# Kernel tuning notes

Hardware: AMD Instinct MI355X
Metric: run time of the kernel (lower is better)

The kernel has to match this reference:

```python
import jax, jax.numpy as jnp
import numpy as np

N_EMBED = 256
N_HEAD = 8
HEAD = N_EMBED // N_HEAD
LN_EPS = 1e-5


def _layernorm(x, g, b):
    mu = jnp.mean(x, axis=-1, keepdims=True)
    var = jnp.mean(jnp.square(x - mu), axis=-1, keepdims=True)
    return (x - mu) * jax.lax.rsqrt(var + LN_EPS) * g + b


def setup_inputs() -> dict:
    key = jax.random.key(0)
    ks = jax.random.split(key, 12)
    B, T, C, H, D = 16, 1024, N_EMBED, N_HEAD, HEAD
    s = C ** -0.5
    return {
        "x": jax.random.normal(ks[0], (B, T, C), jnp.float32),
        "wq": jax.random.normal(ks[1], (H, C, D), jnp.float32) * s,
        "wk": jax.random.normal(ks[2], (H, C, D), jnp.float32) * s,
        "wv": jax.random.normal(ks[3], (H, C, D), jnp.float32) * s,
        "w_proj": jax.random.normal(ks[4], (C, C), jnp.float32) * s,
        "b_proj": jnp.zeros((C,), jnp.float32),
        "w1": jax.random.normal(ks[5], (C, 4 * C), jnp.float32) * s,
        "b1": jnp.zeros((4 * C,), jnp.float32),
        "w2": jax.random.normal(ks[6], (4 * C, C), jnp.float32) * (4 * C) ** -0.5,
        "b2": jnp.zeros((C,), jnp.float32),
        "ln1_g": jnp.ones((C,), jnp.float32),
        "ln1_b": jnp.zeros((C,), jnp.float32),
        "ln2_g": jnp.ones((C,), jnp.float32),
        "ln2_b": jnp.zeros((C,), jnp.float32),
    }


def reference(x, wq, wk, wv, w_proj, b_proj, w1, b1, w2, b2,
              ln1_g, ln1_b, ln2_g, ln2_b):
    B, T, C = x.shape
    # --- multi-head causal self-attention on ln1(x) ---
    h = _layernorm(x, ln1_g, ln1_b)
    q = jnp.einsum('btc,hcd->bhtd', h, wq)
    k = jnp.einsum('btc,hcd->bhtd', h, wk)
    v = jnp.einsum('btc,hcd->bhtd', h, wv)
    # NOTE: original scales by n_embed**-0.5 (C of input), not head_size
    wei = jnp.einsum('bhtd,bhsd->bhts', q, k) * (C ** -0.5)
    causal = jnp.tril(jnp.ones((T, T), bool))
    wei = jnp.where(causal, wei, -jnp.inf)
    wei = jax.nn.softmax(wei, axis=-1)
    att = jnp.einsum('bhts,bhsd->bhtd', wei, v)
    att = att.transpose(0, 2, 1, 3).reshape(B, T, C)  # concat heads
    x = x + att @ w_proj + b_proj
    # --- feedforward on ln2(x) ---
    h2 = _layernorm(x, ln2_g, ln2_b)
    f = jax.nn.relu(h2 @ w1 + b1) @ w2 + b2
    return x + f
```

## Files before the change

kernel.cpp:

```cpp
#include <hip/hip_runtime.h>


typedef unsigned short u16;
typedef unsigned int u32;
typedef __attribute__((ext_vector_type(8))) short short8v;
typedef __attribute__((ext_vector_type(4))) float float4v;

__device__ __forceinline__ float b2f(u16 u) { union { u32 i; float f; } v; v.i = (u32)u << 16; return v.f; }
__device__ __forceinline__ float lo2f(u32 u) { union { u32 i; float f; } v; v.i = u << 16; return v.f; }
__device__ __forceinline__ float hi2f(u32 u) { union { u32 i; float f; } v; v.i = u & 0xffff0000u; return v.f; }
__device__ __forceinline__ u16 f2b(float f) {
    union { float f; u32 i; } v; v.f = f;
    u32 r = v.i + 0x7fffu + ((v.i >> 16) & 1u);
    return (u16)(r >> 16);
}
__device__ __forceinline__ u32 pk2_rtz(float a, float b) {
    return (__float_as_uint(a) >> 16) | (__float_as_uint(b) & 0xffff0000u);
}
__device__ __forceinline__ void async_cp16(const u16* g, u16* l) {
    __builtin_amdgcn_global_load_lds((const __attribute__((address_space(1))) void*)g,
                                     (__attribute__((address_space(3))) void*)l, 16, 0, 0);
}

__global__ __launch_bounds__(256) void prep_ln1(const float* __restrict__ wq,
                                                const float* __restrict__ wk,
                                                const float* __restrict__ wv,
                                                const float* __restrict__ wp,
                                                const float* __restrict__ w1,
                                                const float* __restrict__ w2,
                                                const float* __restrict__ x,
                                                const float* __restrict__ g1,
                                                const float* __restrict__ be1,
                                                u16* __restrict__ wqkvT,
                                                u16* __restrict__ wpT,
                                                u16* __restrict__ w1T,
                                                u16* __restrict__ w2T,
                                                u16* __restrict__ hout) {
    __shared__ u16 tile[64][65];
    int bid = blockIdx.x, tid = threadIdx.x;
    if (bid < 768) {
        int i = bid * 256 + tid;
        int n = i >> 8, k = i & 255;
        int which = n >> 8, nn = n & 255;
        const float* w = which == 0 ? wq : (which == 1 ? wk : wv);
        float v = w[((nn >> 5) * 256 + k) * 32 + (nn & 31)];
        if (which == 0) v *= 0.09016844f;
        wqkvT[i] = f2b(v);
    } else if (bid < 912) {
        const float* src; u16* dst; int K, N, t;
        if (bid < 784)      { src = wp; dst = wpT; K = 256;  N = 256;  t = bid - 768; }
        else if (bid < 848) { src = w1; dst = w1T; K = 256;  N = 1024; t = bid - 784; }
        else                { src = w2; dst = w2T; K = 1024; N = 256;  t = bid - 848; }
        int ntn = N >> 6;
        int k0 = (t / ntn) << 6, n0 = (t % ntn) << 6;
        int lane = tid & 63, wrow = tid >> 6;
        #pragma unroll
        for (int r = 0; r < 16; r++) {
            int k = wrow * 16 + r;
            tile[k][lane] = f2b(src[(size_t)(k0 + k) * N + n0 + lane]);
        }
        __syncthreads();
        #pragma unroll
        for (int r = 0; r < 16; r++) {
            int n = wrow * 16 + r;
            dst[(size_t)(n0 + n) * K + k0 + lane] = tile[lane][n];
        }
    } else {
        int row = (bid - 912) * 4 + (tid >> 6);
        int lane = tid & 63;
        float4 xv = *(const float4*)(x + (size_t)row * 256 + lane * 4);
        float v0 = xv.x, v1 = xv.y, v2 = xv.z, v3 = xv.w;
        float s = v0 + v1 + v2 + v3;
        #pragma unroll
        for (int m = 32; m; m >>= 1) s += __shfl_xor(s, m);
        float mu = s * 0.00390625f;
        float d0 = v0 - mu, d1 = v1 - mu, d2 = v2 - mu, d3 = v3 - mu;
        float ss = d0 * d0 + d1 * d1 + d2 * d2 + d3 * d3;
        #pragma unroll
        for (int m = 32; m; m >>= 1) ss += __shfl_xor(ss, m);
        float rs = rsqrtf(ss * 0.00390625f + 1e-5f);
        float4 g = *(const float4*)(g1 + lane * 4);
        float4 b = *(const float4*)(be1 + lane * 4);
        uint2 r;
        r.x = (u32)f2b(d0 * rs * g.x + b.x) | ((u32)f2b(d1 * rs * g.y + b.y) << 16);
        r.y = (u32)f2b(d2 * rs * g.z + b.z) | ((u32)f2b(d3 * rs * g.w + b.w) << 16);
        *(uint2*)(hout + (size_t)row * 256 + lane * 4) = r;
    }
}

template<bool HASBIAS, bool RELU, bool QKV>
__global__ __launch_bounds__(256) void gemm128(const u16* __restrict__ A,
                                               const u16* __restrict__ Bt,
                                               const float* __restrict__ bias,
                                               u16* __restrict__ out,
                                               u16* __restrict__ vout,
                                               int M, int N, int K) {
    __shared__ __align__(16) u16 SH[17408];
    u16* As = SH;
    u16* Bs = SH + 128 * 64;
    const int tid = threadIdx.x, lane = tid & 63, w = tid >> 6;
    const int m0 = blockIdx.x * 128, n0 = blockIdx.y * 128;
    const int wm = (w & 1) * 64, wn = (w >> 1) * 64;
    const int fm = lane & 15, q = lane >> 4;

    float4v acc[4][4];
    #pragma unroll
    for (int i = 0; i < 4; i++)
        #pragma unroll
        for (int j = 0; j < 4; j++) acc[i][j] = (float4v){0.f, 0.f, 0.f, 0.f};

    const int kset = ((lane & 7) ^ (lane >> 3)) * 8;
    const u16* Ag = A  + (size_t)(m0 + w * 32 + (lane >> 3)) * K + kset;
    const u16* Bg = Bt + (size_t)(n0 + w * 32 + (lane >> 3)) * K + kset;
    u16* Asw = As + (w * 32) * 64;
    u16* Bsw = Bs + (w * 32) * 64;

    const int sw = fm & 7;
    for (int k0 = 0; k0 < K; k0 += 64) {
        __syncthreads();
        #pragma unroll
        for (int c = 0; c < 4; c++) {
            async_cp16(Ag + (size_t)c * 8 * K + k0, Asw + c * 8 * 64);
            async_cp16(Bg + (size_t)c * 8 * K + k0, Bsw + c * 8 * 64);
        }
        __syncthreads();
        #pragma unroll
        for (int kk = 0; kk < 64; kk += 32) {
            const int slot = (((kk >> 3) + q) ^ sw) * 8;
            short8v af[4], bf[4];
            #pragma unroll
            for (int mi = 0; mi < 4; mi++)
                af[mi] = *(const short8v*)&As[(wm + mi * 16 + fm) * 64 + slot];
            #pragma unroll
            for (int ni = 0; ni < 4; ni++)
                bf[ni] = *(const short8v*)&Bs[(wn + ni * 16 + fm) * 64 + slot];
            #pragma unroll
            for (int mi = 0; mi < 4; mi++)
                #pragma unroll
                for (int ni = 0; ni < 4; ni++)
                    acc[mi][ni] = __builtin_amdgcn_mfma_f32_16x16x32_bf16(
                        bf[ni], af[mi], acc[mi][ni], 0, 0, 0);
        }
    }

    if (QKV && n0 >= 512) {
        __syncthreads();
        #pragma unroll
        for (int mi = 0; mi < 4; mi++) {
            int ml = wm + mi * 16 + fm;
            #pragma unroll
            for (int ni = 0; ni < 4; ni++) {
                int nl = wn + ni * 16 + q * 4;
                #pragma unroll
                for (int r = 0; r < 4; r++)
                    SH[(nl + r) * 136 + ml] = f2b(acc[mi][ni][r]);
            }
        }
        __syncthreads();
        int r = tid & 127, c = (tid >> 7) << 6;
        int hd = (n0 - 512) + r;
        int b = m0 >> 10, t0 = m0 & 1023;
        u16* dst = vout + (size_t)(b * 256 + hd) * 1024 + t0 + c;
        const u16* srcT = SH + r * 136 + c;
        #pragma unroll
        for (int i = 0; i < 8; i++)
            *(uint4*)(dst + i * 8) = *(const uint4*)(srcT + i * 8);
        return;
    }

    #pragma unroll
    for (int mi = 0; mi < 4; mi++) {
        int row = m0 + wm + mi * 16 + fm;
        #pragma unroll
        for (int ni = 0; ni < 4; ni++) {
            int nb = n0 + wn + ni * 16 + q * 4;
            float v0 = acc[mi][ni][0], v1 = acc[mi][ni][1],
                  v2 = acc[mi][ni][2], v3 = acc[mi][ni][3];
            if (HASBIAS) {
                float4 bv = *(const float4*)&bias[nb];
                v0 += bv.x; v1 += bv.y; v2 += bv.z; v3 += bv.w;
            }
            if (RELU) {
                v0 = fmaxf(v0, 0.f); v1 = fmaxf(v1, 0.f);
                v2 = fmaxf(v2, 0.f); v3 = fmaxf(v3, 0.f);
            }
            size_t idx = (size_t)row * N + nb;
            uint2 ov;
            ov.x = (u32)f2b(v0) | ((u32)f2b(v1) << 16);
            ov.y = (u32)f2b(v2) | ((u32)f2b(v3) << 16);
            *(uint2*)&out[idx] = ov;
        }
    }
}

__global__ __launch_bounds__(512, 2) void ffn_fused(const u16* __restrict__ h2,
                                                    const u16* __restrict__ w1T,
                                                    const float* __restrict__ b1,
                                                    const u16* __restrict__ w2T,
                                                    const float* __restrict__ b2,
                                                    const u16* __restrict__ x2b,
                                                    float* __restrict__ out) {
    __shared__ __align__(16) u16 SH[65536];
    u16* Ms = SH;
    u16* Bs = SH + 16384;
    const int tid = threadIdx.x, lane = tid & 63, w = tid >> 6;
    const int m0 = blockIdx.x * 64;
    const int wm = (w & 1) * 32;
    const int wn = (w >> 1) * 64;
    const int fm = lane & 15, q = lane >> 4;
    const int sw = fm & 7;
    const int kset = ((lane & 7) ^ (lane >> 3)) * 8;
    const int rb = w * 8 + (lane >> 3);

    short8v ar[8][2];
    {
        const u16* Abase = h2 + (size_t)(m0 + wm + fm) * 256 + q * 8;
        #pragma unroll
        for (int kcn = 0; kcn < 8; kcn++)
            #pragma unroll
            for (int mi = 0; mi < 2; mi++)
                ar[kcn][mi] = *(const short8v*)(Abase + (size_t)mi * 16 * 256 + kcn * 32);
    }

    auto issueB = [&](int t, u16* dst) {
        const int n2 = t >> 3, k2 = t & 3;
        if (((t >> 2) & 1) == 0) {
            const u16* src = w1T + (size_t)(n2 * 256 + rb) * 256 + k2 * 64 + kset;
            #pragma unroll
            for (int c = 0; c < 4; c++)
                async_cp16(src + (size_t)c * 64 * 256, dst + c * 4096);
        } else {
            const u16* src = w2T + (size_t)rb * 1024 + n2 * 256 + k2 * 64 + kset;
            #pragma unroll
            for (int c = 0; c < 4; c++)
                async_cp16(src + (size_t)c * 64 * 1024, dst + c * 4096);
        }
    };

    issueB(0, Bs + w * 512);
    issueB(1, Bs + 16384 + w * 512);

    float4v acc1[2][4], acc2[2][4];
    #pragma unroll
    for (int i = 0; i < 2; i++)
        #pragma unroll
        for (int j = 0; j < 4; j++) acc2[i][j] = (float4v){0.f, 0.f, 0.f, 0.f};

    #pragma unroll
    for (int t = 0; t < 32; ++t) {
        const int nch = t >> 3, ph = (t >> 2) & 1, kc = t & 3;
        if (t == 31) asm volatile("s_waitcnt vmcnt(0)" ::: "memory");
        else         asm volatile("s_waitcnt vmcnt(4)" ::: "memory");
        __builtin_amdgcn_s_barrier();
        if (t + 2 < 32)
            issueB(t + 2, Bs + ((t + 2) % 3) * 16384 + w * 512);
        const u16* Bb = Bs + (t % 3) * 16384;
        if (ph == 0) {
            if (kc == 0) {
                #pragma unroll
                for (int i = 0; i < 2; i++)
                    #pragma unroll
                    for (int j = 0; j < 4; j++) acc1[i][j] = (float4v){0.f, 0.f, 0.f, 0.f};
            }
            #pragma unroll
            for (int kk = 0; kk < 64; kk += 32) {
                const int slot = (((kk >> 3) + q) ^ sw) * 8;
                short8v bf[4];
                #pragma unroll
                for (int ni = 0; ni < 4; ni++)
                    bf[ni] = *(const short8v*)&Bb[(wn + ni * 16 + fm) * 64 + slot];
                #pragma unroll
                for (int mi = 0; mi < 2; mi++)
                    #pragma unroll
                    for (int ni = 0; ni < 4; ni++)
                        acc1[mi][ni] = __builtin_amdgcn_mfma_f32_16x16x32_bf16(
                            bf[ni], ar[kc * 2 + (kk >> 5)][mi], acc1[mi][ni], 0, 0, 0);
            }
            if (kc == 3) {
                #pragma unroll
                for (int ni = 0; ni < 4; ni++) {
                    const int c2 = wn + ni * 16 + q * 4;
                    const int kcM = c2 >> 6, cc = c2 & 63;
                    float4 bv = *(const float4*)&b1[nch * 256 + c2];
                    #pragma unroll
                    for (int mi = 0; mi < 2; mi++) {
                        const int row = wm + mi * 16 + fm;
                        float v0 = fmaxf(acc1[mi][ni][0] + bv.x, 0.f);
                        float v1 = fmaxf(acc1[mi][ni][1] + bv.y, 0.f);
                        float v2 = fmaxf(acc1[mi][ni][2] + bv.z, 0.f);
                        float v3 = fmaxf(acc1[mi][ni][3] + bv.w, 0.f);
                        uint2 pp;
                        pp.x = (u32)f2b(v0) | ((u32)f2b(v1) << 16);
                        pp.y = (u32)f2b(v2) | ((u32)f2b(v3) << 16);
                        *(uint2*)&Ms[kcM * 4096 + row * 64 +
                                     (((cc >> 3) ^ (row & 7)) * 8) + (cc & 7)] = pp;
                    }
                }
                asm volatile("s_waitcnt lgkmcnt(0)" ::: "memory");
            }
        } else {
            const u16* Ab = Ms + kc * 4096;
            #pragma unroll
            for (int kk = 0; kk < 64; kk += 32) {
                const int slot = (((kk >> 3) + q) ^ sw) * 8;
                short8v af[2], bf[4];
                #pragma unroll
                for (int mi = 0; mi < 2; mi++)
                    af[mi] = *(const short8v*)&Ab[(wm + mi * 16 + fm) * 64 + slot];
                #pragma unroll
                for (int ni = 0; ni < 4; ni++)
                    bf[ni] = *(const short8v*)&Bb[(wn + ni * 16 + fm) * 64 + slot];
                #pragma unroll
                for (int mi = 0; mi < 2; mi++)
                    #pragma unroll
                    for (int ni = 0; ni < 4; ni++)
                        acc2[mi][ni] = __builtin_amdgcn_mfma_f32_16x16x32_bf16(
                            bf[ni], af[mi], acc2[mi][ni], 0, 0, 0);
            }
        }
    }

    #pragma unroll
    for (int mi = 0; mi < 2; mi++) {
        const int row = m0 + wm + mi * 16 + fm;
        #pragma unroll
        for (int ni = 0; ni < 4; ni++) {
            const int nb = wn + ni * 16 + q * 4;
            size_t idx = (size_t)row * 256 + nb;
            float4 bv = *(const float4*)&b2[nb];
            uint2 rv = *(const uint2*)&x2b[idx];
            float v0 = acc2[mi][ni][0] + bv.x + lo2f(rv.x);
            float v1 = acc2[mi][ni][1] + bv.y + hi2f(rv.x);
            float v2 = acc2[mi][ni][2] + bv.z + lo2f(rv.y);
            float v3 = acc2[mi][ni][3] + bv.w + hi2f(rv.y);
            *(float4*)&out[idx] = (float4){v0, v1, v2, v3};
        }
    }
}

__global__ __launch_bounds__(256) void proj_ln2(const u16* __restrict__ att,
                                                const u16* __restrict__ wpT,
                                                const float* __restrict__ bp,
                                                const float* __restrict__ x,
                                                const float* __restrict__ g2,
                                                const float* __restrict__ be2,
                                                u16* __restrict__ x2b,
                                                u16* __restrict__ h2) {
    __shared__ __align__(16) u16 As[32 * 64];
    __shared__ __align__(16) u16 Bs[256 * 64];
    __shared__ float gs[256], bs[256], bps[256];
    __shared__ float ps[4][16], pq[4][16];
    const int tid = threadIdx.x, lane = tid & 63, w = tid >> 6;
    const int m0 = blockIdx.x * 32;
    const int wm = (w & 1) * 16, wn = (w >> 1) * 128;
    const int fm = lane & 15, q = lane >> 4;

    gs[tid] = g2[tid]; bs[tid] = be2[tid]; bps[tid] = bp[tid];

    float4v acc[8];
    #pragma unroll
    for (int i = 0; i < 8; i++) acc[i] = (float4v){0.f, 0.f, 0.f, 0.f};

    const int kset = ((lane & 7) ^ (lane >> 3)) * 8;
    const u16* Ag = att + (size_t)(m0 + w * 8 + (lane >> 3)) * 256 + kset;
    const u16* Bg = wpT + (size_t)(w * 64 + (lane >> 3)) * 256 + kset;
    u16* Asw = As + (w * 8) * 64;
    u16* Bsw = Bs + (w * 64) * 64;

    const int sw = fm & 7;
    for (int k0 = 0; k0 < 256; k0 += 64) {
        __syncthreads();
        async_cp16(Ag + k0, Asw);
        #pragma unroll
        for (int c = 0; c < 8; c++)
            async_cp16(Bg + (size_t)c * 8 * 256 + k0, Bsw + c * 8 * 64);
        __syncthreads();
        #pragma unroll
        for (int kk = 0; kk < 64; kk += 32) {
            const int slot = (((kk >> 3) + q) ^ sw) * 8;
            short8v af = *(const short8v*)&As[(wm + fm) * 64 + slot];
            #pragma unroll
            for (int ni = 0; ni < 8; ni++) {
                short8v bf = *(const short8v*)&Bs[(wn + ni * 16 + fm) * 64 + slot];
                acc[ni] = __builtin_amdgcn_mfma_f32_16x16x32_bf16(bf, af, acc[ni], 0, 0, 0);
            }
        }
    }

    int m = m0 + wm + fm;
    float v[8][4];
    float s = 0.f, sq = 0.f;
    #pragma unroll
    for (int ni = 0; ni < 8; ni++) {
        int nb = wn + ni * 16 + q * 4;
        float4 xv = *(const float4*)(x + (size_t)m * 256 + nb);
        float4 bv = *(const float4*)&bps[nb];
        #pragma unroll
        for (int r = 0; r < 4; r++) {
            float t = acc[ni][r] + (&bv.x)[r] + (&xv.x)[r];
            v[ni][r] = t;
            s += t; sq += t * t;
        }
    }
    s += __shfl_xor(s, 16);  s += __shfl_xor(s, 32);
    sq += __shfl_xor(sq, 16); sq += __shfl_xor(sq, 32);
    if (q == 0) { ps[w][fm] = s; pq[w][fm] = sq; }
    __syncthreads();
    s = ps[w][fm] + ps[w ^ 2][fm];
    sq = pq[w][fm] + pq[w ^ 2][fm];
    float mu = s * 0.00390625f;
    float rs = rsqrtf(sq * 0.00390625f - mu * mu + 1e-5f);
    #pragma unroll
    for (int ni = 0; ni < 8; ni++) {
        int nb = wn + ni * 16 + q * 4;
        size_t idx = (size_t)m * 256 + nb;
        float4 gv = *(const float4*)&gs[nb];
        float4 bv = *(const float4*)&bs[nb];
        uint2 xo, ho;
        xo.x = (u32)f2b(v[ni][0]) | ((u32)f2b(v[ni][1]) << 16);
        xo.y = (u32)f2b(v[ni][2]) | ((u32)f2b(v[ni][3]) << 16);
        float h0 = (v[ni][0] - mu) * rs * gv.x + bv.x;
        float h1 = (v[ni][1] - mu) * rs * gv.y + bv.y;
        float h2v = (v[ni][2] - mu) * rs * gv.z + bv.z;
        float h3 = (v[ni][3] - mu) * rs * gv.w + bv.w;
        ho.x = (u32)f2b(h0) | ((u32)f2b(h1) << 16);
        ho.y = (u32)f2b(h2v) | ((u32)f2b(h3) << 16);
        *(uint2*)&x2b[idx] = xo;
        *(uint2*)&h2[idx] = ho;
    }
}

__global__ __launch_bounds__(256) void attn_mfma(const u16* __restrict__ qk,
                                                 const u16* __restrict__ vtg,
                                                 u16* __restrict__ att) {
    const int T = 1024;
    int jj = (blockIdx.x + (blockIdx.y >> 3)) & 7;
    int b = blockIdx.y >> 3, hh = blockIdx.y & 7;
    int tid = threadIdx.x;
    int lane = tid & 63, w = tid >> 6;
    int fm = lane & 15, q = lane >> 4;

    __shared__ __align__(16) u16 Ks[64][72];
    __shared__ __align__(16) u16 Vt[32][72];
    __shared__ __align__(16) u16 Pl[4][16][72];

    size_t base = (size_t)b * T * 512;
    const u16* kb = qk + base + 256 + hh * 32;
    const u16* vt = vtg + (size_t)((b * 8 + hh) * 32) * 1024;
    const int krow = tid >> 2, kcol = (tid & 3) * 8;
    const int vd = tid >> 3, vs = (tid & 7) * 8;

    int qa0 = jj * 64, qb0 = (15 - jj) * 64;
    int tqa = qa0 + w * 16 + fm, tqb = qb0 + w * 16 + fm;
    short8v qfa = *(const short8v*)(qk + base + (size_t)tqa * 512 + hh * 32 + q * 8);
    short8v qfb = *(const short8v*)(qk + base + (size_t)tqb * 512 + hh * 32 + q * 8);
    float4v oa0 = {0.f, 0.f, 0.f, 0.f}, oa1 = {0.f, 0.f, 0.f, 0.f};
    float4v ob0 = {0.f, 0.f, 0.f, 0.f}, ob1 = {0.f, 0.f, 0.f, 0.f};
    float la = 0.f, lb = 0.f;
    int wqa = qa0 + w * 16, wqb = qb0 + w * 16;
    int nIter = 16 - jj;

    uint4 kreg = *(const uint4*)(kb + (size_t)krow * 512 + kcol);
    uint4 vreg = *(const uint4*)(vt + (size_t)vd * 1024 + vs);

    for (int it = 0; it < nIter; ++it) {
        int s0 = it << 6;
        __syncthreads();
        *(uint4*)&Ks[krow][kcol] = kreg;
        *(uint4*)&Vt[vd][vs] = vreg;
        __syncthreads();
        if (it + 1 < nIter) {
            int ns0 = s0 + 64;
            kreg = *(const uint4*)(kb + (size_t)(ns0 + krow) * 512 + kcol);
            vreg = *(const uint4*)(vt + (size_t)vd * 1024 + ns0 + vs);
        }
        short8v kf0 = *(const short8v*)&Ks[fm][q * 8];
        short8v kf1 = *(const short8v*)&Ks[16 + fm][q * 8];
        short8v kf2 = *(const short8v*)&Ks[32 + fm][q * 8];
        short8v kf3 = *(const short8v*)&Ks[48 + fm][q * 8];
        short8v vf00 = *(const short8v*)&Vt[fm][q * 8];
        short8v vf01 = *(const short8v*)&Vt[fm][32 + q * 8];
        short8v vf10 = *(const short8v*)&Vt[16 + fm][q * 8];
        short8v vf11 = *(const short8v*)&Vt[16 + fm][32 + q * 8];
        float4v z = {0.f, 0.f, 0.f, 0.f};

        #pragma unroll
        for (int t2 = 0; t2 < 2; t2++) {
            int wq0 = t2 ? wqa : wqb;
            if (s0 >= wq0 + 16) continue;
            int tq = t2 ? tqa : tqb;
            short8v qf = t2 ? qfa : qfb;
            float4v s_0 = __builtin_amdgcn_mfma_f32_16x16x32_bf16(kf0, qf, z, 0, 0, 0);
            float4v s_1 = __builtin_amdgcn_mfma_f32_16x16x32_bf16(kf1, qf, z, 0, 0, 0);
            float4v s_2 = __builtin_amdgcn_mfma_f32_16x16x32_bf16(kf2, qf, z, 0, 0, 0);
            float4v s_3 = __builtin_amdgcn_mfma_f32_16x16x32_bf16(kf3, qf, z, 0, 0, 0);
            float p[16];
            #pragma unroll
            for (int r = 0; r < 4; r++) {
                p[r] = exp2f(s_0[r]); p[4 + r] = exp2f(s_1[r]);
                p[8 + r] = exp2f(s_2[r]); p[12 + r] = exp2f(s_3[r]);
            }
            if (s0 + 63 > wq0) {
                int sb = s0 + q * 4;
                #pragma unroll
                for (int c = 0; c < 4; c++)
                    #pragma unroll
                    for (int r = 0; r < 4; r++)
                        if (sb + c * 16 + r > tq) p[c * 4 + r] = 0.f;
            }
            float rsum = 0.f;
            #pragma unroll
            for (int i = 0; i < 16; i++) rsum += p[i];
            rsum += __shfl_xor(rsum, 16);
            rsum += __shfl_xor(rsum, 32);
            if (t2) la += rsum; else lb += rsum;

            #pragma unroll
            for (int c = 0; c < 4; c++) {
                uint2 pp;
                pp.x = pk2_rtz(p[c * 4 + 0], p[c * 4 + 1]);
                pp.y = pk2_rtz(p[c * 4 + 2], p[c * 4 + 3]);
                *(uint2*)&Pl[w][fm][c * 16 + q * 4] = pp;
            }
            short8v pf0 = *(const short8v*)&Pl[w][fm][q * 8];
            short8v pf1 = *(const short8v*)&Pl[w][fm][32 + q * 8];
            if (t2) {
                oa0 = __builtin_amdgcn_mfma_f32_16x16x32_bf16(vf00, pf0, oa0, 0, 0, 0);
                oa0 = __builtin_amdgcn_mfma_f32_16x16x32_bf16(vf01, pf1, oa0, 0, 0, 0);
                oa1 = __builtin_amdgcn_mfma_f32_16x16x32_bf16(vf10, pf0, oa1, 0, 0, 0);
                oa1 = __builtin_amdgcn_mfma_f32_16x16x32_bf16(vf11, pf1, oa1, 0, 0, 0);
            } else {
                ob0 = __builtin_amdgcn_mfma_f32_16x16x32_bf16(vf00, pf0, ob0, 0, 0, 0);
                ob0 = __builtin_amdgcn_mfma_f32_16x16x32_bf16(vf01, pf1, ob0, 0, 0, 0);
                ob1 = __builtin_amdgcn_mfma_f32_16x16x32_bf16(vf10, pf0, ob1, 0, 0, 0);
                ob1 = __builtin_amdgcn_mfma_f32_16x16x32_bf16(vf11, pf1, ob1, 0, 0, 0);
            }
        }
    }

    #pragma unroll
    for (int t2 = 0; t2 < 2; t2++) {
        float inv = 1.f / (t2 ? la : lb);
        float4v o0 = t2 ? oa0 : ob0, o1 = t2 ? oa1 : ob1;
        int tq = t2 ? tqa : tqb;
        uint2 r0, r1;
        r0.x = (u32)f2b(o0[0] * inv) | ((u32)f2b(o0[1] * inv) << 16);
        r0.y = (u32)f2b(o0[2] * inv) | ((u32)f2b(o0[3] * inv) << 16);
        r1.x = (u32)f2b(o1[0] * inv) | ((u32)f2b(o1[1] * inv) << 16);
        r1.y = (u32)f2b(o1[2] * inv) | ((u32)f2b(o1[3] * inv) << 16);
        size_t o = (size_t)(b * T + tq) * 256 + hh * 32;
        *(uint2*)(att + o + q * 4) = r0;
        *(uint2*)(att + o + 16 + q * 4) = r1;
    }
}

extern "C" void kernel_launch(void* const* d_in, const int* in_sizes, int n_in,
                              void* d_out, int out_size, void* d_ws, size_t ws_size,
                              hipStream_t stream) {
    const int BT = 16 * 1024;
    const float* x      = (const float*)d_in[0];
    const float* wq     = (const float*)d_in[1];
    const float* wk     = (const float*)d_in[2];
    const float* wv     = (const float*)d_in[3];
    const float* w_proj = (const float*)d_in[4];
    const float* b_proj = (const float*)d_in[5];
    const float* w1     = (const float*)d_in[6];
    const float* b1     = (const float*)d_in[7];
    const float* w2     = (const float*)d_in[8];
    const float* b2     = (const float*)d_in[9];
    const float* ln1_g  = (const float*)d_in[10];
    const float* ln1_b  = (const float*)d_in[11];
    const float* ln2_g  = (const float*)d_in[12];
    const float* ln2_b  = (const float*)d_in[13];

    char* ws = (char*)d_ws;
    const size_t MB = 1024 * 1024;
    u16*  x2b   = (u16*)(ws + 0);
    u16*  hbuf  = (u16*)(ws + 8 * MB);
    u16*  qk    = (u16*)(ws + 16 * MB);
    u16*  vtg   = (u16*)(ws + 32 * MB);
    u16*  wqkvT = (u16*)(ws + 48 * MB);
    u16*  wpT   = (u16*)(ws + 48 * MB + 0x60000);
    u16*  w1T   = (u16*)(ws + 48 * MB + 0x80000);
    u16*  w2T   = (u16*)(ws + 48 * MB + 0x100000);

    prep_ln1<<<5008, 256, 0, stream>>>(wq, wk, wv, w_proj, w1, w2, x, ln1_g, ln1_b,
                                       wqkvT, wpT, w1T, w2T, hbuf);
    gemm128<false, false, true><<<dim3(128, 6), 256, 0, stream>>>(
        hbuf, wqkvT, nullptr, qk, vtg, BT, 512, 256);
    attn_mfma<<<dim3(8, 128), 256, 0, stream>>>(qk, vtg, hbuf);
    proj_ln2<<<512, 256, 0, stream>>>(hbuf, wpT, b_proj, x, ln2_g, ln2_b, x2b, hbuf);
    ffn_fused<<<256, 512, 0, stream>>>(hbuf, w1T, b1, w2T, b2, x2b, (float*)d_out);
}
```

Measured before the change: 178.7 us.

## Double-buffer LDS tiles with async prefetch in gemm128 and proj_ln2

Both GEMM kernels now use two LDS buffers and issue the global-to-LDS async copies for tile t+2 while tile t is being computed. Each step waits with partial vmcnt counts instead of draining all loads behind two full barriers. The K loop is hard-coded to four 64-wide steps, so it assumes K=256. LDS use per block roughly doubles, which may lower occupancy. proj_ln2 also stops staging gamma, beta and bias in shared memory and reads them straight from global memory in the epilogue.

After: 178.5 us. Within noise of the previous version (-0.1%).

```diff
diff --git a/kernel.cpp b/kernel.cpp
--- a/kernel.cpp
+++ b/kernel.cpp
@@ -95,9 +95,7 @@
                                                u16* __restrict__ out,
                                                u16* __restrict__ vout,
                                                int M, int N, int K) {
-    __shared__ __align__(16) u16 SH[17408];
-    u16* As = SH;
-    u16* Bs = SH + 128 * 64;
+    __shared__ __align__(16) u16 SH[32768];
     const int tid = threadIdx.x, lane = tid & 63, w = tid >> 6;
     const int m0 = blockIdx.x * 128, n0 = blockIdx.y * 128;
     const int wm = (w & 1) * 64, wn = (w >> 1) * 64;
@@ -112,18 +110,27 @@
     const int kset = ((lane & 7) ^ (lane >> 3)) * 8;
     const u16* Ag = A  + (size_t)(m0 + w * 32 + (lane >> 3)) * K + kset;
     const u16* Bg = Bt + (size_t)(n0 + w * 32 + (lane >> 3)) * K + kset;
-    u16* Asw = As + (w * 32) * 64;
-    u16* Bsw = Bs + (w * 32) * 64;
+
+    auto issueS = [&](int t, int d) {
+        u16* Asw = SH + d * 16384 + (w * 32) * 64;
+        u16* Bsw = SH + d * 16384 + 8192 + (w * 32) * 64;
+        #pragma unroll
+        for (int c = 0; c < 4; c++) {
+            async_cp16(Ag + (size_t)c * 8 * K + t * 64, Asw + c * 8 * 64);
+            async_cp16(Bg + (size_t)c * 8 * K + t * 64, Bsw + c * 8 * 64);
+        }
+    };
+    issueS(0, 0);
+    issueS(1, 1);
 
     const int sw = fm & 7;
-    for (int k0 = 0; k0 < K; k0 += 64) {
-        __syncthreads();
-        #pragma unroll
-        for (int c = 0; c < 4; c++) {
-            async_cp16(Ag + (size_t)c * 8 * K + k0, Asw + c * 8 * 64);
-            async_cp16(Bg + (size_t)c * 8 * K + k0, Bsw + c * 8 * 64);
-        }
-        __syncthreads();
+    #pragma unroll
+    for (int t = 0; t < 4; ++t) {
+        if (t == 3) asm volatile("s_waitcnt vmcnt(0)" ::: "memory");
+        else        asm volatile("s_waitcnt vmcnt(8)" ::: "memory");
+        __builtin_amdgcn_s_barrier();
+        const u16* As = SH + (t & 1) * 16384;
+        const u16* Bs = As + 8192;
         #pragma unroll
         for (int kk = 0; kk < 64; kk += 32) {
             const int slot = (((kk >> 3) + q) ^ sw) * 8;
@@ -140,6 +147,10 @@
                 for (int ni = 0; ni < 4; ni++)
                     acc[mi][ni] = __builtin_amdgcn_mfma_f32_16x16x32_bf16(
                         bf[ni], af[mi], acc[mi][ni], 0, 0, 0);
+        }
+        if (t < 2) {
+            __builtin_amdgcn_s_barrier();
+            issueS(t + 2, t & 1);
         }
     }
 
@@ -346,17 +357,13 @@
                                                 const float* __restrict__ be2,
                                                 u16* __restrict__ x2b,
                                                 u16* __restrict__ h2) {
-    __shared__ __align__(16) u16 As[32 * 64];
-    __shared__ __align__(16) u16 Bs[256 * 64];
-    __shared__ float gs[256], bs[256], bps[256];
+    __shared__ __align__(16) u16 AB[2][18432];
     __shared__ float ps[4][16], pq[4][16];
     const int tid = threadIdx.x, lane = tid & 63, w = tid >> 6;
     const int m0 = blockIdx.x * 32;
     const int wm = (w & 1) * 16, wn = (w >> 1) * 128;
     const int fm = lane & 15, q = lane >> 4;
 
-    gs[tid] = g2[tid]; bs[tid] = be2[tid]; bps[tid] = bp[tid];
-
     float4v acc[8];
     #pragma unroll
     for (int i = 0; i < 8; i++) acc[i] = (float4v){0.f, 0.f, 0.f, 0.f};
@@ -364,17 +371,26 @@
     const int kset = ((lane & 7) ^ (lane >> 3)) * 8;
     const u16* Ag = att + (size_t)(m0 + w * 8 + (lane >> 3)) * 256 + kset;
     const u16* Bg = wpT + (size_t)(w * 64 + (lane >> 3)) * 256 + kset;
-    u16* Asw = As + (w * 8) * 64;
-    u16* Bsw = Bs + (w * 64) * 64;
+
+    auto issueS = [&](int t, int d) {
+        u16* Asw = AB[d] + (w * 8) * 64;
+        u16* Bsw = AB[d] + 2048 + (w * 64) * 64;
+        async_cp16(Ag + t * 64, Asw);
+        #pragma unroll
+        for (int c = 0; c < 8; c++)
+            async_cp16(Bg + (size_t)c * 8 * 256 + t * 64, Bsw + c * 8 * 64);
+    };
+    issueS(0, 0);
+    issueS(1, 1);
 
     const int sw = fm & 7;
-    for (int k0 = 0; k0 < 256; k0 += 64) {
-        __syncthreads();
-        async_cp16(Ag + k0, Asw);
-        #pragma unroll
-        for (int c = 0; c < 8; c++)
-            async_cp16(Bg + (size_t)c * 8 * 256 + k0, Bsw + c * 8 * 64);
-        __syncthreads();
+    #pragma unroll
+    for (int t = 0; t < 4; ++t) {
+        if (t == 3) asm volatile("s_waitcnt vmcnt(0)" ::: "memory");
+        else        asm volatile("s_waitcnt vmcnt(9)" ::: "memory");
+        __builtin_amdgcn_s_barrier();
+        const u16* As = AB[t & 1];
+        const u16* Bs = AB[t & 1] + 2048;
         #pragma unroll
         for (int kk = 0; kk < 64; kk += 32) {
             const int slot = (((kk >> 3) + q) ^ sw) * 8;
@@ -385,6 +401,10 @@
                 acc[ni] = __builtin_amdgcn_mfma_f32_16x16x32_bf16(bf, af, acc[ni], 0, 0, 0);
             }
         }
+        if (t < 2) {
+            __builtin_amdgcn_s_barrier();
+            issueS(t + 2, t & 1);
+        }
     }
 
     int m = m0 + wm + fm;
@@ -394,7 +414,7 @@
     for (int ni = 0; ni < 8; ni++) {
         int nb = wn + ni * 16 + q * 4;
         float4 xv = *(const float4*)(x + (size_t)m * 256 + nb);
-        float4 bv = *(const float4*)&bps[nb];
+        float4 bv = *(const float4*)&bp[nb];
         #pragma unroll
         for (int r = 0; r < 4; r++) {
             float t = acc[ni][r] + (&bv.x)[r] + (&xv.x)[r];
@@ -414,8 +434,8 @@
     for (int ni = 0; ni < 8; ni++) {
         int nb = wn + ni * 16 + q * 4;
         size_t idx = (size_t)m * 256 + nb;
-        float4 gv = *(const float4*)&gs[nb];
-        float4 bv = *(const float4*)&bs[nb];
+        float4 gv = *(const float4*)&g2[nb];
+        float4 bv = *(const float4*)&be2[nb];
         uint2 xo, ho;
         xo.x = (u32)f2b(v[ni][0]) | ((u32)f2b(v[ni][1]) << 16);
         xo.y = (u32)f2b(v[ni][2]) | ((u32)f2b(v[ni][3]) << 16);
```
